# Kernel optimization log

Measured on AMD Instinct MI355X. Metric: run time of the kernel, lower is better.

## Reference

```python
import jax, jax.numpy as jnp
import numpy as np
from jax import lax

D = 4            # shift radius
NSHIFT = 2 * D + 1  # 9 shifts per axis -> 81 total


def setup_inputs() -> dict:
    key = jax.random.key(0)
    k1, k2, k3, k4, k5, k6 = jax.random.split(key, 6)
    B, C, H, W = 4, 256, 64, 128
    R = 16  # reduction ratio
    feat1 = jax.random.normal(k1, (B, C, H, W), dtype=jnp.float32)
    feat2 = jax.random.normal(k2, (B, C, H, W), dtype=jnp.float32)
    # ca_conv1: Conv2d(C, C//R, 1) -> weight [C//R, C], bias [C//R]
    w1 = jax.random.normal(k3, (C // R, C), dtype=jnp.float32) * (1.0 / np.sqrt(C))
    b1 = jax.random.normal(k4, (C // R,), dtype=jnp.float32) * 0.01
    # ca_conv2: Conv2d(C//R, C, 1) -> weight [C, C//R], bias [C]
    w2 = jax.random.normal(k5, (C, C // R), dtype=jnp.float32) * (1.0 / np.sqrt(C // R))
    b2 = jax.random.normal(k6, (C,), dtype=jnp.float32) * 0.01
    return {"feat1": feat1, "feat2": feat2, "w1": w1, "b1": b1, "w2": w2, "b2": b2}


def reference(feat1, feat2, w1, b1, w2, b2):
    B, C, H, W = feat1.shape
    # zero-pad feat2 spatially by D on each side (matches F.pad constant 0)
    feat2p = jnp.pad(feat2, ((0, 0), (0, 0), (D, D), (D, D)))

    def one_shift(carry, idx):
        i = idx // NSHIFT
        j = idx % NSHIFT
        f2 = lax.dynamic_slice(feat2p, (0, 0, i, j), (B, C, H, W))
        sim = feat1 * f2                              # [B,C,H,W]
        pooled = jnp.mean(sim, axis=(2, 3))           # global avg pool -> [B,C]
        a = pooled @ w1.T + b1                        # [B,C//R] (1x1 conv == matmul)
        a = a @ w2.T + b2                             # [B,C]
        a = jax.nn.sigmoid(a)
        out = jnp.mean(a[:, :, None, None] * sim, axis=1)  # channel mean -> [B,H,W]
        return carry, out

    _, cv = lax.scan(one_shift, None, jnp.arange(NSHIFT * NSHIFT))  # [81,B,H,W]
    return jnp.transpose(cv, (1, 0, 2, 3))  # [B,81,H,W]
```

## Files before the change

kernel.cpp:

```cpp
#include <hip/hip_runtime.h>
#include <math.h>


#define HH 64
#define WW 128
#define CC 256
#define BB 4

typedef float v2f __attribute__((ext_vector_type(2)));

__global__ __launch_bounds__(576) void corr_pool_kernel(
    const float* __restrict__ f1, const float* __restrict__ f2,
    float* __restrict__ pooled) {
  const int t  = threadIdx.x;
  const int bc = blockIdx.x;
  const float* f1p = f1 + (size_t)bc * (HH * WW);
  const float* f2p = f2 + (size_t)bc * (HH * WW);

  __shared__ float4 f2s4[72 * 35];

  const float4 z4 = make_float4(0.f, 0.f, 0.f, 0.f);
  for (int u = t; u < 72 * 35; u += 576) {
    const int rl = u / 35, k = u - rl * 35;
    const int gr = rl - 4;
    float4 v = z4;
    if ((unsigned)gr < 64u && k >= 1 && k <= 32)
      v = *(const float4*)(f2p + (gr << 7) + ((k - 1) << 2));
    f2s4[u] = v;
  }
  __syncthreads();

  const int h  = t / 9;
  const int di = t - h * 9;
  const float4* f2row = &f2s4[(h + di) * 35];
  const float* f1row  = f1p + (h << 7);

  float s9[9];
#pragma unroll
  for (int j = 0; j < 9; ++j) s9[j] = 0.f;

  alignas(16) float f1c[16], f2wc[24];
#pragma unroll
  for (int m = 0; m < 4; ++m)
    *(float4*)&f1c[4 * m] = *(const float4*)(f1row + (m << 2));
#pragma unroll
  for (int m = 0; m < 6; ++m) *(float4*)&f2wc[4 * m] = f2row[m];

  for (int seg = 0; seg < 8; ++seg) {
    const int nxt = (seg < 7) ? seg + 1 : 7;
    alignas(16) float f1n[16], f2wn[24];
#pragma unroll
    for (int m = 0; m < 4; ++m)
      *(float4*)&f1n[4 * m] =
          *(const float4*)(f1row + (nxt << 4) + (m << 2));
#pragma unroll
    for (int m = 0; m < 6; ++m) *(float4*)&f2wn[4 * m] = f2row[(nxt << 2) + m];

#pragma unroll
    for (int k = 0; k < 16; ++k) {
      const float a = f1c[k];
#pragma unroll
      for (int j = 0; j < 9; ++j) s9[j] += a * f2wc[k + j];
    }
#pragma unroll
    for (int m = 0; m < 16; ++m) f1c[m] = f1n[m];
#pragma unroll
    for (int m = 0; m < 24; ++m) f2wc[m] = f2wn[m];
  }

  __syncthreads();
  float* red  = (float*)f2s4;
  float* red2 = red + 64 * 81;
#pragma unroll
  for (int j = 0; j < 9; ++j) red[h * 81 + di * 9 + j] = s9[j];
  __syncthreads();

  if (t < 567) {
    const int col = t % 81, g = t / 81;
    const int r0 = g * 9, r1 = (g == 6) ? 64 : r0 + 9;
    float acc = 0.f;
#pragma unroll 3
    for (int rr = r0; rr < r1; ++rr) acc += red[rr * 81 + col];
    red2[g * 81 + col] = acc;
  }
  __syncthreads();

  if (t < 81) {
    float acc = 0.f;
#pragma unroll
    for (int g = 0; g < 7; ++g) acc += red2[g * 81 + t];
    const int b = bc >> 8, c = bc & 255;
    pooled[(size_t)(b * 81 + t) * 256 + c] = acc;
  }
}

__global__ __launch_bounds__(256) void mlp_kernel(
    const float* __restrict__ pooled, const float* __restrict__ w1,
    const float* __restrict__ b1, const float* __restrict__ w2,
    const float* __restrict__ b2, float* __restrict__ At) {
  const int bs = blockIdx.x;
  const int t  = threadIdx.x;
  const int b  = bs / 81;
  const int s  = bs - b * 81;
  __shared__ float p[256];
  __shared__ float hid[16];

  p[t] = pooled[(size_t)bs * 256 + t] * (1.0f / 8192.0f);
  __syncthreads();

  const int g = t >> 4, ln = t & 15;
  float acc = 0.f;
#pragma unroll
  for (int m = 0; m < 16; ++m) {
    const int c = (m << 4) + ln;
    acc += w1[(g << 8) + c] * p[c];
  }
  acc += __shfl_xor(acc, 1);
  acc += __shfl_xor(acc, 2);
  acc += __shfl_xor(acc, 4);
  acc += __shfl_xor(acc, 8);
  if (ln == 0) hid[g] = acc + b1[g];
  __syncthreads();

  float acc2 = b2[t];
#pragma unroll
  for (int k = 0; k < 16; ++k) acc2 += w2[(t << 4) + k] * hid[k];
  const float sv = 1.0f / (1.0f + __expf(-acc2));
  At[((size_t)(b * 256 + t)) * 81 + s] = sv;
}

__device__ __forceinline__ void async16(const float* g, void* lds) {
  __builtin_amdgcn_global_load_lds(
      (const __attribute__((address_space(1))) void*)g,
      (__attribute__((address_space(3))) void*)lds, 16, 0, 0);
}

__global__ __launch_bounds__(576) void out_kernel(
    const float* __restrict__ f1, const float* __restrict__ f2,
    const float* __restrict__ At, float* __restrict__ out,
    float* __restrict__ part) {
  const int bid  = blockIdx.x;
  const int work = (bid & 7) * 32 + (bid >> 3);
  const int rt   = work & 31;
  const int half = (work >> 5) & 1;
  const int b    = work >> 6;
  const int h0   = rt << 1;

  const int t    = threadIdx.x;
  const int wv   = t >> 6;
  const int lane = t & 63;
  const int r    = lane >> 5;
  const int cidx = lane & 31;
  const int w0   = cidx << 2;
  const int h    = h0 + r;
  const int iu   = __builtin_amdgcn_readfirstlane(wv);

  __shared__ float4 st[2][2][12][32];
  __shared__ float4 trash[64];

  const int c0 = half << 7;
  const float* f1pl = f1 + ((size_t)b * 256 + c0) * 8192;
  const float* f2pl = f2 + ((size_t)b * 256 + c0) * 8192;
  const float* Aa   = At + ((size_t)(b * 256 + c0)) * 81 + iu * 9;

  const int chA   = (wv >= 6) ? 1 : 0;
  const int slotA = wv - 6 * chA;
  const bool isF1A = (slotA == 5);
  const int prowA  = h0 - 4 + 2 * slotA;
  const bool validA = isF1A || ((unsigned)prowA < 63u);
  const int crowA  = isF1A ? h0 : ((prowA < 0) ? 0 : ((prowA > 62) ? 62 : prowA));
  const float* gA = (isF1A ? f1pl : f2pl) + crowA * 128 +
                    (size_t)chA * 8192 + lane * 4;
  float4* dA0 = validA ? &st[0][chA][2 * slotA][0] : &trash[0];
  float4* dA1 = validA ? &st[1][chA][2 * slotA][0] : &trash[0];

  const bool hasB  = (wv < 3);
  const int slotB  = (hasB ? wv : 0) + 3;
  const bool isF1B = (slotB == 5);
  const int prowB  = h0 - 4 + 2 * slotB;
  const bool validB = hasB && (isF1B || ((unsigned)prowB < 63u));
  const int crowB  = isF1B ? h0 : ((prowB < 0) ? 0 : ((prowB > 62) ? 62 : prowB));
  const float* gB = (isF1B ? f1pl : f2pl) + crowB * 128 +
                    (size_t)8192 + lane * 4;
  float4* dB0 = validB ? &st[0][1][2 * slotB][0] : &trash[0];
  float4* dB1 = validB ? &st[1][1][2 * slotB][0] : &trash[0];

  {
    const float4 z4 = make_float4(0.f, 0.f, 0.f, 0.f);
    float4* stf = &st[0][0][0][0];
    for (int u = t; u < 2 * 2 * 12 * 32; u += 576) stf[u] = z4;
  }
  __syncthreads();

  async16(gA, dA0);
  async16(gB, dB0);

  v2f acc2[9][2];
#pragma unroll
  for (int j = 0; j < 9; ++j) {
    acc2[j][0] = (v2f)(0.f);
    acc2[j][1] = (v2f)(0.f);
  }

  const bool vA = (cidx > 0);
  const bool vC = (cidx < 31);
  const int cxm1 = vA ? cidx - 1 : cidx;
  const int cxp1 = vC ? cidx + 1 : cidx;
  const int riu  = r + iu;

  for (int k = 0; k < 64; ++k) {
    const int cur = k & 1;

    const int adv = (k < 63) ? 16384 : 0;
    gA += adv; gB += adv;
    float4* dA = cur ? dA0 : dA1;
    float4* dB = cur ? dB0 : dB1;
    async16(gA, dA);
    async16(gB, dB);

    asm volatile("s_waitcnt vmcnt(2)" ::: "memory");
    __builtin_amdgcn_s_barrier();

    const float* ca = Aa + (size_t)(2 * k) * 81;
#pragma unroll
    for (int sub = 0; sub < 2; ++sub) {
      const float* cf = ca + sub * 81;
      const float4 x4 = st[cur][sub][10 + r][cidx];
      const float4 A4 = st[cur][sub][riu][cxm1];
      const float4 B4 = st[cur][sub][riu][cidx];
      const float4 C4 = st[cur][sub][riu][cxp1];

      alignas(16) float f2r[12];
      f2r[0]  = vA ? A4.x : 0.f;
      f2r[1]  = vA ? A4.y : 0.f;
      f2r[2]  = vA ? A4.z : 0.f;
      f2r[3]  = vA ? A4.w : 0.f;
      f2r[4]  = B4.x; f2r[5] = B4.y; f2r[6] = B4.z; f2r[7] = B4.w;
      f2r[8]  = vC ? C4.x : 0.f;
      f2r[9]  = vC ? C4.y : 0.f;
      f2r[10] = vC ? C4.z : 0.f;
      f2r[11] = vC ? C4.w : 0.f;

      const v2f xx01 = {x4.x, x4.y};
      const v2f xx23 = {x4.z, x4.w};

#pragma unroll
      for (int j = 0; j < 9; ++j) {
        const float wj = cf[j];
        const v2f w2  = {wj, wj};
        const v2f p01 = {f2r[j],     f2r[j + 1]};
        const v2f p23 = {f2r[j + 2], f2r[j + 3]};
        acc2[j][0] += w2 * (xx01 * p01);
        acc2[j][1] += w2 * (xx23 * p23);
      }
    }

    __builtin_amdgcn_s_barrier();
  }

  asm volatile("s_waitcnt vmcnt(0)" ::: "memory");

  float* dst = half ? part : out;
  const float inv = 1.0f / 256.0f;
#pragma unroll
  for (int j = 0; j < 9; ++j) {
    float4 o;
    o.x = acc2[j][0].x * inv;
    o.y = acc2[j][0].y * inv;
    o.z = acc2[j][1].x * inv;
    o.w = acc2[j][1].y * inv;
    *(float4*)(dst + (((size_t)(b * 81 + iu * 9 + j) * 64 + h) << 7) + w0) = o;
  }
}

__global__ __launch_bounds__(256) void combine_kernel(
    float* __restrict__ out, const float* __restrict__ part) {
  const size_t idx = (size_t)blockIdx.x * 256 + threadIdx.x;
  float4* o4       = (float4*)out;
  const float4* p4 = (const float4*)part;
  const float4 a = o4[idx], p = p4[idx];
  float4 rv;
  rv.x = a.x + p.x; rv.y = a.y + p.y; rv.z = a.z + p.z; rv.w = a.w + p.w;
  o4[idx] = rv;
}

extern "C" void kernel_launch(void* const* d_in, const int* in_sizes, int n_in,
                              void* d_out, int out_size, void* d_ws, size_t ws_size,
                              hipStream_t stream) {
  const float* feat1 = (const float*)d_in[0];
  const float* feat2 = (const float*)d_in[1];
  const float* w1    = (const float*)d_in[2];
  const float* b1    = (const float*)d_in[3];
  const float* w2    = (const float*)d_in[4];
  const float* b2    = (const float*)d_in[5];
  float* out = (float*)d_out;

  float* pooled = (float*)d_ws;
  float* At     = pooled + 82944;
  float* cpart  = At + 82944;

  corr_pool_kernel<<<1024, 576, 0, stream>>>(feat1, feat2, pooled);
  mlp_kernel<<<4 * 81, 256, 0, stream>>>(pooled, w1, b1, w2, b2, At);
  out_kernel<<<256, 576, 0, stream>>>(feat1, feat2, At, out, cpart);
  combine_kernel<<<2592, 256, 0, stream>>>(out, cpart);
}
```

Baseline: 216.7 us.

## Replace async global-to-LDS loads with register prefetch and stage coefficients in LDS

Replaces the direct global_load_lds double-buffer pipeline with plain register loads of the next tile, issued before compute and written to the alternate LDS buffer after compute, with one __syncthreads per iteration. It also preloads all 128x81 attention coefficients for the block into LDS, so the inner loop reads them from shared memory instead of global/scalar memory. This trades the async-copy path and its waitcnt handling for register staging, adds about 41KB of LDS per block (which may limit occupancy), and adds an upfront coefficient load.

```diff
diff --git a/kernel.cpp b/kernel.cpp
--- a/kernel.cpp
+++ b/kernel.cpp
@@ -129,12 +129,6 @@
   At[((size_t)(b * 256 + t)) * 81 + s] = sv;
 }
 
-__device__ __forceinline__ void async16(const float* g, void* lds) {
-  __builtin_amdgcn_global_load_lds(
-      (const __attribute__((address_space(1))) void*)g,
-      (__attribute__((address_space(3))) void*)lds, 16, 0, 0);
-}
-
 __global__ __launch_bounds__(576) void out_kernel(
     const float* __restrict__ f1, const float* __restrict__ f2,
     const float* __restrict__ At, float* __restrict__ out,
@@ -156,12 +150,12 @@
   const int iu   = __builtin_amdgcn_readfirstlane(wv);
 
   __shared__ float4 st[2][2][12][32];
-  __shared__ float4 trash[64];
+  __shared__ float coefL[128 * 81];
 
   const int c0 = half << 7;
   const float* f1pl = f1 + ((size_t)b * 256 + c0) * 8192;
   const float* f2pl = f2 + ((size_t)b * 256 + c0) * 8192;
-  const float* Aa   = At + ((size_t)(b * 256 + c0)) * 81 + iu * 9;
+  const float* Atb  = At + ((size_t)(b * 256 + c0)) * 81;
 
   const int chA   = (wv >= 6) ? 1 : 0;
   const int slotA = wv - 6 * chA;
@@ -171,8 +165,7 @@
   const int crowA  = isF1A ? h0 : ((prowA < 0) ? 0 : ((prowA > 62) ? 62 : prowA));
   const float* gA = (isF1A ? f1pl : f2pl) + crowA * 128 +
                     (size_t)chA * 8192 + lane * 4;
-  float4* dA0 = validA ? &st[0][chA][2 * slotA][0] : &trash[0];
-  float4* dA1 = validA ? &st[1][chA][2 * slotA][0] : &trash[0];
+  const int rowA_lds = isF1A ? (10) : (2 * slotA);
 
   const bool hasB  = (wv < 3);
   const int slotB  = (hasB ? wv : 0) + 3;
@@ -182,8 +175,7 @@
   const int crowB  = isF1B ? h0 : ((prowB < 0) ? 0 : ((prowB > 62) ? 62 : prowB));
   const float* gB = (isF1B ? f1pl : f2pl) + crowB * 128 +
                     (size_t)8192 + lane * 4;
-  float4* dB0 = validB ? &st[0][1][2 * slotB][0] : &trash[0];
-  float4* dB1 = validB ? &st[1][1][2 * slotB][0] : &trash[0];
+  const int rowB_lds = isF1B ? (10) : (2 * slotB);
 
   {
     const float4 z4 = make_float4(0.f, 0.f, 0.f, 0.f);
@@ -192,8 +184,15 @@
   }
   __syncthreads();
 
-  async16(gA, dA0);
-  async16(gB, dB0);
+  for (int u = t; u < 128 * 81; u += 576) coefL[u] = Atb[u];
+
+  {
+    const float4 vA0 = *(const float4*)(gA);
+    const float4 vB0 = *(const float4*)(gB);
+    if (validA) (&st[0][chA][rowA_lds][0])[lane] = vA0;
+    if (validB) (&st[0][1][rowB_lds][0])[lane] = vB0;
+  }
+  __syncthreads();
 
   v2f acc2[9][2];
 #pragma unroll
@@ -209,22 +208,16 @@
   const int riu  = r + iu;
 
   for (int k = 0; k < 64; ++k) {
-    const int cur = k & 1;
+    const int cur = k & 1, nxt = cur ^ 1;
 
     const int adv = (k < 63) ? 16384 : 0;
     gA += adv; gB += adv;
-    float4* dA = cur ? dA0 : dA1;
-    float4* dB = cur ? dB0 : dB1;
-    async16(gA, dA);
-    async16(gB, dB);
-
-    asm volatile("s_waitcnt vmcnt(2)" ::: "memory");
-    __builtin_amdgcn_s_barrier();
-
-    const float* ca = Aa + (size_t)(2 * k) * 81;
+    const float4 vAn = *(const float4*)(gA);
+    const float4 vBn = *(const float4*)(gB);
+
 #pragma unroll
     for (int sub = 0; sub < 2; ++sub) {
-      const float* cf = ca + sub * 81;
+      const float* cf = coefL + (size_t)(2 * k + sub) * 81 + iu * 9;
       const float4 x4 = st[cur][sub][10 + r][cidx];
       const float4 A4 = st[cur][sub][riu][cxm1];
       const float4 B4 = st[cur][sub][riu][cidx];
@@ -255,10 +248,11 @@
       }
     }
 
-    __builtin_amdgcn_s_barrier();
-  }
-
-  asm volatile("s_waitcnt vmcnt(0)" ::: "memory");
+    if (validA) (&st[nxt][chA][rowA_lds][0])[lane] = vAn;
+    if (validB) (&st[nxt][1][rowB_lds][0])[lane] = vBn;
+
+    __syncthreads();
+  }
 
   float* dst = half ? part : out;
   const float inv = 1.0f / 256.0f;
```

Result: faster. 206.1 us (-4.9%).
